# Optimization experiments

Measured on AMD Instinct MI355X. Metric: run time of the kernel, lower is better.

## Reference

```python
import jax, jax.numpy as jnp
import numpy as np

N_NODES = 100000
N_EDGES = 640000
D = 128


def setup_inputs() -> dict:
    key = jax.random.key(0)
    k1, k2, k3 = jax.random.split(key, 3)
    h = jax.random.normal(k1, (N_NODES, D), dtype=jnp.float32)
    edges = jax.random.randint(k2, (2, N_EDGES), 0, N_NODES, dtype=jnp.int64)
    W = jax.random.normal(k3, (1, D), dtype=jnp.float32) / np.sqrt(D)
    b = jnp.zeros((1,), dtype=jnp.float32)
    return {"h": h, "edges": edges, "W": W, "b": b}


def reference(h, edges, W, b):
    # gather source/object node features: [E, D]
    s = h[edges[0]]
    o = h[edges[1]]
    # tiny linear on fused elementwise sin(s - o): [E, 1]
    score = jnp.sin(s - o) @ W.T + b
    # pairwise softmax over consecutive edge pairs (torch F.softmax dim=1 on [E/2, 2])
    score = jax.nn.softmax(score.reshape(-1, 2), axis=1).reshape(-1, 1)
    return (score, score > 0.5)
```

## Files before the change

### kernel.cpp

```cpp
#include <hip/hip_runtime.h>


__global__ __launch_bounds__(256) void sine_predictor_kernel(
    const float* __restrict__ h,
    const int*   __restrict__ edges,
    const float* __restrict__ W,
    const float* __restrict__ b,
    float*       __restrict__ out,
    int n_edges)
{
    const int lane = threadIdx.x & 63;
    const int sub  = lane & 31;
    const int half = lane >> 5;
    const int waves_per_block = blockDim.x >> 6;
    const int wave_in_block   = threadIdx.x >> 6;
    const int n_pairs = n_edges >> 1;

    const float4 w4  = reinterpret_cast<const float4*>(W)[sub];
    const float bias = b[0];

    int pair = blockIdx.x * waves_per_block + wave_in_block;
    const int stride = gridDim.x * waves_per_block;

    for (; pair < n_pairs; pair += stride) {
        const int e   = 2 * pair + half;
        const int src = edges[e];
        const int obj = edges[n_edges + e];

        const float4 s4 = reinterpret_cast<const float4*>(h + (size_t)src * 128)[sub];
        const float4 o4 = reinterpret_cast<const float4*>(h + (size_t)obj * 128)[sub];

        float part = sinf(s4.x - o4.x) * w4.x
                   + sinf(s4.y - o4.y) * w4.y
                   + sinf(s4.z - o4.z) * w4.z
                   + sinf(s4.w - o4.w) * w4.w;

        #pragma unroll
        for (int m = 16; m >= 1; m >>= 1)
            part += __shfl_xor(part, m, 64);

        const float x     = part + bias;
        const float other = __shfl_xor(x, 32, 64);
        const float mx    = fmaxf(x, other);
        const float es    = __expf(x - mx);
        const float eo    = __expf(other - mx);
        const float p     = es / (es + eo);

        if (sub == 0) {
            out[e]           = p;
            out[n_edges + e] = (p > 0.5f) ? 1.0f : 0.0f;
        }
    }
}

extern "C" void kernel_launch(void* const* d_in, const int* in_sizes, int n_in,
                              void* d_out, int out_size, void* d_ws, size_t ws_size,
                              hipStream_t stream) {
    const float* h     = (const float*)d_in[0];
    const int*   edges = (const int*)d_in[1];
    const float* W     = (const float*)d_in[2];
    const float* b     = (const float*)d_in[3];
    float*       out   = (float*)d_out;

    const int n_edges = in_sizes[1] / 2;

    const int blocks = 2048;
    sine_predictor_kernel<<<blocks, 256, 0, stream>>>(h, edges, W, b, out, n_edges);
}
```

Measured before the change: 98.98 us.

## Bucket-sort edges by source node before gathering, and split softmax into own pass

```diff
diff --git a/kernel.cpp b/kernel.cpp
--- a/kernel.cpp
+++ b/kernel.cpp
@@ -1,7 +1,128 @@
 #include <hip/hip_runtime.h>
 
 
-__global__ __launch_bounds__(256) void sine_predictor_kernel(
+constexpr int DIMS      = 128;
+constexpr int NB        = 4096;
+constexpr int KEY_SHIFT = 5;
+
+using u32 = unsigned int;
+
+__global__ __launch_bounds__(1024) void zero_hist_kernel(u32* __restrict__ hist) {
+    const int t = blockIdx.x * blockDim.x + threadIdx.x;
+    if (t < NB) hist[t] = 0u;
+}
+
+__global__ __launch_bounds__(256) void hist_kernel(
+    const int* __restrict__ edges, int E, u32* __restrict__ hist)
+{
+    int i = blockIdx.x * blockDim.x + threadIdx.x;
+    const int stride = gridDim.x * blockDim.x;
+    for (; i < E; i += stride)
+        atomicAdd(&hist[((u32)edges[i]) >> KEY_SHIFT], 1u);
+}
+
+__global__ __launch_bounds__(1024) void prefix_kernel(
+    const u32* __restrict__ hist, u32* __restrict__ cursor)
+{
+    __shared__ u32 sums[1024];
+    const int t = threadIdx.x;
+    const u32 h0 = hist[4*t+0], h1 = hist[4*t+1], h2 = hist[4*t+2], h3 = hist[4*t+3];
+    const u32 s  = h0 + h1 + h2 + h3;
+    sums[t] = s;
+    __syncthreads();
+    for (int d = 1; d < 1024; d <<= 1) {
+        const u32 v = (t >= d) ? sums[t-d] : 0u;
+        __syncthreads();
+        sums[t] += v;
+        __syncthreads();
+    }
+    const u32 excl = sums[t] - s;
+    cursor[4*t+0] = excl;
+    cursor[4*t+1] = excl + h0;
+    cursor[4*t+2] = excl + h0 + h1;
+    cursor[4*t+3] = excl + h0 + h1 + h2;
+}
+
+__global__ __launch_bounds__(256) void scatter_kernel(
+    const int* __restrict__ edges, int E, u32* __restrict__ cursor,
+    uint2* __restrict__ order)
+{
+    int i = blockIdx.x * blockDim.x + threadIdx.x;
+    const int stride = gridDim.x * blockDim.x;
+    for (; i < E; i += stride) {
+        const u32 src = (u32)edges[i];
+        const u32 obj = (u32)edges[E + i];
+        const u32 pos = atomicAdd(&cursor[src >> KEY_SHIFT], 1u);
+        order[pos] = make_uint2(src | ((u32)(i & 0x7FFF) << 17),
+                                obj | ((u32)(i >> 15) << 17));
+    }
+}
+
+__global__ __launch_bounds__(256) void score_sorted_kernel(
+    const float* __restrict__ h,
+    const uint2* __restrict__ order,
+    const float* __restrict__ W,
+    float*       __restrict__ xbuf,
+    int E)
+{
+    const int lane    = threadIdx.x & 63;
+    const int sub     = lane & 15;
+    const int quarter = lane >> 4;
+    const int wave_id = blockIdx.x * (blockDim.x >> 6) + (threadIdx.x >> 6);
+    const int n_waves = gridDim.x * (blockDim.x >> 6);
+    const int span    = (E + n_waves - 1) / n_waves;
+    const int start   = wave_id * span;
+    const int end     = min(E, start + span);
+
+    const float4 wl = reinterpret_cast<const float4*>(W)[sub * 2 + 0];
+    const float4 wh = reinterpret_cast<const float4*>(W)[sub * 2 + 1];
+
+    for (int ib = start; ib < end; ib += 4) {
+        const int  i     = ib + quarter;
+        const bool valid = i < end;
+        const int  ic    = valid ? i : end - 1;
+
+        const uint2 ent = order[ic];
+        const u32 src = ent.x & 0x1FFFFu;
+        const u32 obj = ent.y & 0x1FFFFu;
+        const u32 e   = (ent.x >> 17) | ((ent.y >> 17) << 15);
+
+        const float4* sr = reinterpret_cast<const float4*>(h + (size_t)src * DIMS);
+        const float4* om = reinterpret_cast<const float4*>(h + (size_t)obj * DIMS);
+        const float4 s0 = sr[sub * 2 + 0];
+        const float4 s1 = sr[sub * 2 + 1];
+        const float4 o0 = om[sub * 2 + 0];
+        const float4 o1 = om[sub * 2 + 1];
+
+        float x = __sinf(s0.x - o0.x) * wl.x + __sinf(s0.y - o0.y) * wl.y
+                + __sinf(s0.z - o0.z) * wl.z + __sinf(s0.w - o0.w) * wl.w
+                + __sinf(s1.x - o1.x) * wh.x + __sinf(s1.y - o1.y) * wh.y
+                + __sinf(s1.z - o1.z) * wh.z + __sinf(s1.w - o1.w) * wh.w;
+
+        #pragma unroll
+        for (int m = 8; m >= 1; m >>= 1) x += __shfl_xor(x, m, 64);
+
+        if (sub == 0 && valid) xbuf[e] = x;
+    }
+}
+
+__global__ __launch_bounds__(256) void softmax_kernel(
+    const float* __restrict__ xbuf, float* __restrict__ out, int E)
+{
+    const int NP = E >> 1;
+    int p = blockIdx.x * blockDim.x + threadIdx.x;
+    const int stride = gridDim.x * blockDim.x;
+    for (; p < NP; p += stride) {
+        const float2 x  = reinterpret_cast<const float2*>(xbuf)[p];
+        const float  p0 = 1.0f / (1.0f + __expf(x.y - x.x));
+        const float  p1 = 1.0f / (1.0f + __expf(x.x - x.y));
+        reinterpret_cast<float2*>(out)[p]     = make_float2(p0, p1);
+        reinterpret_cast<float2*>(out + E)[p] =
+            make_float2(p0 > 0.5f ? 1.0f : 0.0f, p1 > 0.5f ? 1.0f : 0.0f);
+    }
+}
+
+__global__ __launch_bounds__(256, 6) void sine_predictor_fp32_kernel(
     const float* __restrict__ h,
     const int*   __restrict__ edges,
     const float* __restrict__ W,
@@ -9,44 +130,38 @@
     float*       __restrict__ out,
     int n_edges)
 {
-    const int lane = threadIdx.x & 63;
-    const int sub  = lane & 31;
-    const int half = lane >> 5;
-    const int waves_per_block = blockDim.x >> 6;
-    const int wave_in_block   = threadIdx.x >> 6;
-    const int n_pairs = n_edges >> 1;
-
-    const float4 w4  = reinterpret_cast<const float4*>(W)[sub];
+    const int lane    = threadIdx.x & 63;
+    const int sub     = lane & 15;
+    const int quarter = lane >> 4;
+    const int wave_id = blockIdx.x * (blockDim.x >> 6) + (threadIdx.x >> 6);
+    const int n_waves = gridDim.x * (blockDim.x >> 6);
+    const int n_ch    = (n_edges + 3) >> 2;
+
+    const float4 wl  = reinterpret_cast<const float4*>(W)[sub * 2 + 0];
+    const float4 wh  = reinterpret_cast<const float4*>(W)[sub * 2 + 1];
     const float bias = b[0];
 
-    int pair = blockIdx.x * waves_per_block + wave_in_block;
-    const int stride = gridDim.x * waves_per_block;
-
-    for (; pair < n_pairs; pair += stride) {
-        const int e   = 2 * pair + half;
-        const int src = edges[e];
-        const int obj = edges[n_edges + e];
-
-        const float4 s4 = reinterpret_cast<const float4*>(h + (size_t)src * 128)[sub];
-        const float4 o4 = reinterpret_cast<const float4*>(h + (size_t)obj * 128)[sub];
-
-        float part = sinf(s4.x - o4.x) * w4.x
-                   + sinf(s4.y - o4.y) * w4.y
-                   + sinf(s4.z - o4.z) * w4.z
-                   + sinf(s4.w - o4.w) * w4.w;
-
+    for (int c = wave_id; c < n_ch; c += n_waves) {
+        const int e  = 4 * c + quarter;
+        const int ec = min(e, n_edges - 1);
+        const int src = edges[ec];
+        const int obj = edges[n_edges + ec];
+        const float4* sr = reinterpret_cast<const float4*>(h + (size_t)src * DIMS);
+        const float4* om = reinterpret_cast<const float4*>(h + (size_t)obj * DIMS);
+        const float4 s0 = sr[sub * 2 + 0];
+        const float4 s1 = sr[sub * 2 + 1];
+        const float4 o0 = om[sub * 2 + 0];
+        const float4 o1 = om[sub * 2 + 1];
+        float x = __sinf(s0.x - o0.x) * wl.x + __sinf(s0.y - o0.y) * wl.y
+                + __sinf(s0.z - o0.z) * wl.z + __sinf(s0.w - o0.w) * wl.w
+                + __sinf(s1.x - o1.x) * wh.x + __sinf(s1.y - o1.y) * wh.y
+                + __sinf(s1.z - o1.z) * wh.z + __sinf(s1.w - o1.w) * wh.w;
         #pragma unroll
-        for (int m = 16; m >= 1; m >>= 1)
-            part += __shfl_xor(part, m, 64);
-
-        const float x     = part + bias;
-        const float other = __shfl_xor(x, 32, 64);
-        const float mx    = fmaxf(x, other);
-        const float es    = __expf(x - mx);
-        const float eo    = __expf(other - mx);
-        const float p     = es / (es + eo);
-
-        if (sub == 0) {
+        for (int m = 8; m >= 1; m >>= 1) x += __shfl_xor(x, m, 64);
+        x += bias;
+        const float other = __shfl_xor(x, 16, 64);
+        const float p = 1.0f / (1.0f + __expf(other - x));
+        if (sub == 0 && e < n_edges) {
             out[e]           = p;
             out[n_edges + e] = (p > 0.5f) ? 1.0f : 0.0f;
         }
@@ -63,7 +178,26 @@
     float*       out   = (float*)d_out;
 
     const int n_edges = in_sizes[1] / 2;
-
-    const int blocks = 2048;
-    sine_predictor_kernel<<<blocks, 256, 0, stream>>>(h, edges, W, b, out, n_edges);
-}
+    const int n_nodes = in_sizes[0] / DIMS;
+
+    const size_t off_cursor = (size_t)NB * 4;
+    const size_t off_order  = off_cursor + (size_t)NB * 4;
+    const size_t off_xbuf   = off_order + (size_t)n_edges * 8;
+    const size_t need       = off_xbuf + (size_t)n_edges * 4;
+
+    if (ws_size >= need && n_nodes <= (NB << KEY_SHIFT) && (n_edges & 1) == 0) {
+        u32*   hist   = (u32*)d_ws;
+        u32*   cursor = (u32*)((char*)d_ws + off_cursor);
+        uint2* order  = (uint2*)((char*)d_ws + off_order);
+        float* xbuf   = (float*)((char*)d_ws + off_xbuf);
+
+        zero_hist_kernel<<<(NB + 1023) / 1024, 1024, 0, stream>>>(hist);
+        hist_kernel<<<1024, 256, 0, stream>>>(edges, n_edges, hist);
+        prefix_kernel<<<1, 1024, 0, stream>>>(hist, cursor);
+        scatter_kernel<<<1024, 256, 0, stream>>>(edges, n_edges, cursor, order);
+        score_sorted_kernel<<<2048, 256, 0, stream>>>(h, order, W, xbuf, n_edges);
+        softmax_kernel<<<512, 256, 0, stream>>>(xbuf, out, n_edges);
+    } else {
+        sine_predictor_fp32_kernel<<<1536, 256, 0, stream>>>(h, edges, W, b, out, n_edges);
+    }
+}
```

After: 212.7 us. +114.9%, slower.

## Process four edges per wave with 16 lanes each and fast sine intrinsics

Applied to the files above, without the earlier changes.

```diff
diff --git a/kernel.cpp b/kernel.cpp
--- a/kernel.cpp
+++ b/kernel.cpp
@@ -1,7 +1,9 @@
 #include <hip/hip_runtime.h>
 
 
-__global__ __launch_bounds__(256) void sine_predictor_kernel(
+constexpr int DIMS = 128;
+
+__global__ __launch_bounds__(256, 6) void sine_predictor_kernel(
     const float* __restrict__ h,
     const int*   __restrict__ edges,
     const float* __restrict__ W,
@@ -9,44 +11,42 @@
     float*       __restrict__ out,
     int n_edges)
 {
-    const int lane = threadIdx.x & 63;
-    const int sub  = lane & 31;
-    const int half = lane >> 5;
-    const int waves_per_block = blockDim.x >> 6;
-    const int wave_in_block   = threadIdx.x >> 6;
-    const int n_pairs = n_edges >> 1;
+    const int lane    = threadIdx.x & 63;
+    const int sub     = lane & 15;
+    const int quarter = lane >> 4;
+    const int wave_id = blockIdx.x * (blockDim.x >> 6) + (threadIdx.x >> 6);
+    const int n_waves = gridDim.x * (blockDim.x >> 6);
+    const int n_ch    = (n_edges + 3) >> 2;
 
-    const float4 w4  = reinterpret_cast<const float4*>(W)[sub];
+    const float4 wl  = reinterpret_cast<const float4*>(W)[sub * 2 + 0];
+    const float4 wh  = reinterpret_cast<const float4*>(W)[sub * 2 + 1];
     const float bias = b[0];
 
-    int pair = blockIdx.x * waves_per_block + wave_in_block;
-    const int stride = gridDim.x * waves_per_block;
+    for (int c = wave_id; c < n_ch; c += n_waves) {
+        const int e  = 4 * c + quarter;
+        const int ec = min(e, n_edges - 1);
+        const int src = edges[ec];
+        const int obj = edges[n_edges + ec];
 
-    for (; pair < n_pairs; pair += stride) {
-        const int e   = 2 * pair + half;
-        const int src = edges[e];
-        const int obj = edges[n_edges + e];
+        const float4* sr = reinterpret_cast<const float4*>(h + (size_t)src * DIMS);
+        const float4* om = reinterpret_cast<const float4*>(h + (size_t)obj * DIMS);
+        const float4 s0 = sr[sub * 2 + 0];
+        const float4 s1 = sr[sub * 2 + 1];
+        const float4 o0 = om[sub * 2 + 0];
+        const float4 o1 = om[sub * 2 + 1];
 
-        const float4 s4 = reinterpret_cast<const float4*>(h + (size_t)src * 128)[sub];
-        const float4 o4 = reinterpret_cast<const float4*>(h + (size_t)obj * 128)[sub];
-
-        float part = sinf(s4.x - o4.x) * w4.x
-                   + sinf(s4.y - o4.y) * w4.y
-                   + sinf(s4.z - o4.z) * w4.z
-                   + sinf(s4.w - o4.w) * w4.w;
+        float x = __sinf(s0.x - o0.x) * wl.x + __sinf(s0.y - o0.y) * wl.y
+                + __sinf(s0.z - o0.z) * wl.z + __sinf(s0.w - o0.w) * wl.w
+                + __sinf(s1.x - o1.x) * wh.x + __sinf(s1.y - o1.y) * wh.y
+                + __sinf(s1.z - o1.z) * wh.z + __sinf(s1.w - o1.w) * wh.w;
 
         #pragma unroll
-        for (int m = 16; m >= 1; m >>= 1)
-            part += __shfl_xor(part, m, 64);
+        for (int m = 8; m >= 1; m >>= 1) x += __shfl_xor(x, m, 64);
+        x += bias;
 
-        const float x     = part + bias;
-        const float other = __shfl_xor(x, 32, 64);
-        const float mx    = fmaxf(x, other);
-        const float es    = __expf(x - mx);
-        const float eo    = __expf(other - mx);
-        const float p     = es / (es + eo);
-
-        if (sub == 0) {
+        const float other = __shfl_xor(x, 16, 64);
+        const float p = 1.0f / (1.0f + __expf(other - x));
+        if (sub == 0 && e < n_edges) {
             out[e]           = p;
             out[n_edges + e] = (p > 0.5f) ? 1.0f : 0.0f;
         }
@@ -64,6 +64,5 @@
 
     const int n_edges = in_sizes[1] / 2;
 
-    const int blocks = 2048;
-    sine_predictor_kernel<<<blocks, 256, 0, stream>>>(h, edges, W, b, out, n_edges);
+    sine_predictor_kernel<<<1536, 256, 0, stream>>>(h, edges, W, b, out, n_edges);
 }
```

Result: faster. 92.40 us (-6.6%).
